# Kernel optimization log

Measured on AMD Instinct MI355X. Metric: run time of the kernel, lower is better.

The kernel has to match this reference:

```python
import jax, jax.numpy as jnp
import numpy as np

NUM_LAYERS = 3
H = 128          # hidden_dim
COMP_DIM = 128
PROT_DIM = 128
EPS = 1e-6


def setup_inputs() -> dict:
    key = jax.random.key(0)
    ks = jax.random.split(key, 20)
    B, Lc, Lp = 16, 512, 4096
    s = 0.05
    inp = {
        "comp_feat": jax.random.normal(ks[0], (B, Lc, COMP_DIM), jnp.float32),
        "comp_mask": jax.random.randint(ks[1], (B, Lc), 0, 2, jnp.int32),
        "prot_feat": jax.random.normal(ks[2], (B, Lp, PROT_DIM), jnp.float32),
        "prot_mask": jax.random.randint(ks[3], (B, Lp), 0, 2, jnp.int32),
        # per-layer params, stacked on leading layer axis. Linear(x) = x @ W + b
        # (W stored already transposed relative to torch's [out,in] layout).
        "Wc": jax.random.normal(ks[4], (NUM_LAYERS, COMP_DIM, H), jnp.float32) * s,
        "bc": jnp.zeros((NUM_LAYERS, H), jnp.float32),
        "Wp": jax.random.normal(ks[5], (NUM_LAYERS, PROT_DIM, H), jnp.float32) * s,
        "bp": jnp.zeros((NUM_LAYERS, H), jnp.float32),
        "Wbl": jax.random.normal(ks[6], (NUM_LAYERS, H, H), jnp.float32) * s,  # bilinear, no bias
        "Wac": jax.random.normal(ks[7], (NUM_LAYERS, H), jnp.float32) * s,    # Linear(H,1) weight
        "bac": jnp.zeros((NUM_LAYERS,), jnp.float32),
        "Wap": jax.random.normal(ks[8], (NUM_LAYERS, H), jnp.float32) * s,
        "bap": jnp.zeros((NUM_LAYERS,), jnp.float32),
        "Wcomb_c": jax.random.normal(ks[9], (NUM_LAYERS * H, H), jnp.float32) * s,
        "bcomb_c": jnp.zeros((H,), jnp.float32),
        "Wcomb_p": jax.random.normal(ks[10], (NUM_LAYERS * H, H), jnp.float32) * s,
        "bcomb_p": jnp.zeros((H,), jnp.float32),
    }
    return inp


def _masked_softmax(scores, mask):
    # faithful to torch: max over ALL entries (mask applied post-exp), +1e-6 denom
    m = jnp.max(scores, axis=-1, keepdims=True)
    e = jnp.exp(scores - m) * mask
    return e / (jnp.sum(e, axis=-1, keepdims=True) + EPS)


def reference(comp_feat, comp_mask, prot_feat, prot_mask,
              Wc, bc, Wp, bp, Wbl, Wac, bac, Wap, bap,
              Wcomb_c, bcomb_c, Wcomb_p, bcomb_p):
    cm = comp_mask.astype(jnp.float32)  # [B,Lc]
    pm = prot_mask.astype(jnp.float32)  # [B,Lp]
    comp_pooled_list, prot_pooled_list = [], []
    comp_context = prot_context = None
    for i in range(NUM_LAYERS):
        comp_proj = jnp.tanh(comp_feat @ Wc[i] + bc[i])   # [B,Lc,H]
        prot_proj = jnp.tanh(prot_feat @ Wp[i] + bp[i])   # [B,Lp,H]
        comp_bil = comp_proj @ Wbl[i]                      # [B,Lc,H]
        scores = jnp.einsum('bqh,bkh->bqk', comp_bil, prot_proj)  # [B,Lc,Lp]
        scores = scores * (cm[:, :, None] * pm[:, None, :])
        # broadcast-multiply-sum in torch == matmul; same math, efficient form
        comp_context = jnp.einsum('bqk,bkh->bqh', scores, prot_proj)  # [B,Lc,H]
        prot_context = jnp.einsum('bqk,bqh->bkh', scores, comp_proj)  # [B,Lp,H]
        cw = _masked_softmax(comp_context @ Wac[i] + bac[i], cm)  # [B,Lc]
        pw = _masked_softmax(prot_context @ Wap[i] + bap[i], pm)  # [B,Lp]
        comp_pooled_list.append(jnp.einsum('bqh,bq->bh', comp_proj, cw))
        prot_pooled_list.append(jnp.einsum('bkh,bk->bh', prot_proj, pw))
    comp_final = jnp.concatenate(comp_pooled_list, axis=1) @ Wcomb_c + bcomb_c
    prot_final = jnp.concatenate(prot_pooled_list, axis=1) @ Wcomb_p + bcomb_p
    # contexts returned are from the last layer (matches torch loop-variable leak)
    return (comp_final, prot_final, comp_context, prot_context)
```

## Files before the change

### kernel.cpp

```cpp
#include <hip/hip_runtime.h>
#include <math.h>

#define B_ 16
#define LC_ 512
#define LP_ 4096
#define H_ 128
#define HH_ (H_*H_)

typedef unsigned long long u64t;
typedef unsigned short u16t;
typedef __attribute__((ext_vector_type(8))) short bf16x8;
typedef __attribute__((ext_vector_type(4))) float f32x4;

__device__ __forceinline__ u16t f2bf(float f) {
    union { float f; unsigned u; } v; v.f = f;
    unsigned r = (v.u + 0x7FFFu + ((v.u >> 16) & 1u)) >> 16;
    return (u16t)r;
}
__device__ __forceinline__ float bf2f(u16t s) {
    union { unsigned u; float f; } v; v.u = ((unsigned)s) << 16; return v.f;
}
__device__ __forceinline__ float bflo(unsigned u) {
    union { unsigned u; float f; } v; v.u = u << 16; return v.f;
}
__device__ __forceinline__ float bfhi(unsigned u) {
    union { unsigned u; float f; } v; v.u = u & 0xffff0000u; return v.f;
}
__device__ __forceinline__ unsigned cvtpk2(float a, float b) {
    unsigned r;
    asm volatile("v_cvt_pk_bf16_f32 %0, %1, %2" : "=v"(r) : "v"(a), "v"(b));
    return r;
}
__device__ __forceinline__ float ftanh(float x) {
    float e = __expf(2.f * x);
    return fmaf(-2.f, __builtin_amdgcn_rcpf(e + 1.f), 1.f);
}
__device__ __forceinline__ bf16x8 ldfragS(const short* base, int r, int k, int stride) {
    const u64t* p = (const u64t*)(base + (size_t)r * stride + k);
    union { bf16x8 v; u64t q[2]; } u;
    u.q[0] = p[0]; u.q[1] = p[1];
    return u.v;
}
__device__ __forceinline__ bf16x8 ldfragG(const u16t* p) {
    union { bf16x8 v; uint4 q; } u;
    u.q = *(const uint4*)p;
    return u.v;
}

__device__ __forceinline__ void wprep_body(const float* __restrict__ src,
                                           u16t* __restrict__ h, u16t* __restrict__ l,
                                           int t) {
    const int n = t >> 1, k0 = (t & 1) * 64;
#pragma unroll 4
    for (int k = 0; k < 64; ++k) {
        float v = src[(size_t)(k0 + k) * H_ + n];
        u16t hh = f2bf(v);
        h[(size_t)n * H_ + k0 + k] = hh;
        l[(size_t)n * H_ + k0 + k] = f2bf(v - bf2f(hh));
    }
}

__global__ __launch_bounds__(256) void prep_k(const float* __restrict__ s0,
                                              const float* __restrict__ s1,
                                              const float* __restrict__ s2,
                                              u16t* __restrict__ hi, u16t* __restrict__ lo,
                                              float* __restrict__ zcp,
                                              float* __restrict__ zout) {
    const int bid = blockIdx.x, t = threadIdx.x;
    if (bid < 9) {
        const int grp = bid / 3, lay = bid % 3;
        const float* src = (grp == 0 ? s0 : grp == 1 ? s1 : s2) + (size_t)lay * HH_;
        wprep_body(src, hi + (size_t)bid * HH_, lo + (size_t)bid * HH_, t);
    } else {
        float4 zero = make_float4(0.f, 0.f, 0.f, 0.f);
        float4* z = (float4*)zcp;
        for (int j = t; j < 3072; j += 256) z[j] = zero;
        float4* z2 = (float4*)zout;
        for (int j = t; j < 1024; j += 256) z2[j] = zero;
    }
}

template<int ROWS>
__device__ __forceinline__ void stage_fp32(const float* __restrict__ X,
                                           short* __restrict__ Xs, int t) {
#pragma unroll
    for (int j = 0; j < ROWS / 16; ++j) {
        int lin = j * 512 + t;
        int row = lin >> 5, c4 = lin & 31;
        float4 v = ((const float4*)X)[lin];
        u64t pk = (u64t)cvtpk2(v.x, v.y) | ((u64t)cvtpk2(v.z, v.w) << 32);
        *(u64t*)(Xs + (size_t)row * 136 + c4 * 4) = pk;
    }
}
__device__ __forceinline__ void stage_bf16(const u16t* __restrict__ X,
                                           short* __restrict__ Xs, int t) {
#pragma unroll
    for (int j = 0; j < 4; ++j) {
        int lin = j * 512 + t;
        *(uint4*)(Xs + (lin >> 4) * 136 + (lin & 15) * 8) = ((const uint4*)X)[lin];
    }
}

template<int NRG, bool TANH, bool BF16OUT, bool LDSOUT>
__device__ __forceinline__ void gemm_core(const short* __restrict__ Xs,
                                          const u16t* __restrict__ Whi,
                                          const u16t* __restrict__ Wlo,
                                          const float* __restrict__ bias,
                                          const int* __restrict__ mrow,
                                          void* __restrict__ Yrow0,
                                          short* __restrict__ projLds, int t) {
    const int l = t & 63, w = t >> 6;
    const int lm = l & 15, lk = (l >> 4) * 8, lr = (l >> 4) * 4;
    const int wcol = w * 16;
    const size_t wrow = (size_t)(wcol + lm) * H_;
    f32x4 acc[NRG] = {};
#pragma unroll
    for (int ks = 0; ks < 128; ks += 32) {
        bf16x8 ah = ldfragG(Whi + wrow + ks + lk);
        bf16x8 al = ldfragG(Wlo + wrow + ks + lk);
#pragma unroll
        for (int rg = 0; rg < NRG; ++rg) {
            bf16x8 xb = ldfragS(Xs, rg * 16 + lm, ks + lk, 136);
            acc[rg] = __builtin_amdgcn_mfma_f32_16x16x32_bf16(ah, xb, acc[rg], 0, 0, 0);
            acc[rg] = __builtin_amdgcn_mfma_f32_16x16x32_bf16(al, xb, acc[rg], 0, 0, 0);
        }
    }
    if (LDSOUT) __syncthreads();
    const int col = wcol + lr;
    float4 bq = make_float4(0.f, 0.f, 0.f, 0.f);
    if (bias) bq = *(const float4*)(bias + col);
#pragma unroll
    for (int rg = 0; rg < NRG; ++rg) {
        const int row = rg * 16 + lm;
        float v0 = acc[rg][0] + bq.x, v1 = acc[rg][1] + bq.y;
        float v2 = acc[rg][2] + bq.z, v3 = acc[rg][3] + bq.w;
        if (TANH) { v0 = ftanh(v0); v1 = ftanh(v1); v2 = ftanh(v2); v3 = ftanh(v3); }
        if (mrow) {
            const float msc = (float)mrow[row];
            v0 *= msc; v1 *= msc; v2 *= msc; v3 *= msc;
        }
        if (BF16OUT) {
            u64t pk = (u64t)cvtpk2(v0, v1) | ((u64t)cvtpk2(v2, v3) << 32);
            *(u64t*)((u16t*)Yrow0 + (size_t)row * H_ + col) = pk;
            if (LDSOUT) *(u64t*)(projLds + (size_t)row * 136 + col) = pk;
        } else {
            float4 o; o.x = v0; o.y = v1; o.z = v2; o.w = v3;
            *(float4*)((float*)Yrow0 + (size_t)row * H_ + col) = o;
        }
    }
}

__global__ __launch_bounds__(512) void gemmB_k(const float* __restrict__ prot_feat,
                                               const float* __restrict__ comp_feat,
                                               const u16t* __restrict__ WHi,
                                               const u16t* __restrict__ WLo,
                                               const float* __restrict__ bp,
                                               const float* __restrict__ bc,
                                               u16t* __restrict__ prot_proj,
                                               u16t* __restrict__ comp_proj,
                                               u16t* __restrict__ comp_bil) {
    extern __shared__ __align__(16) short smem[];
    const int t = threadIdx.x, bx = blockIdx.x;
    if (bx < 128) {
        short* Xs = smem;
        short* Ys = smem + 64 * 136;
        const long row0 = (long)bx * 64;
        stage_fp32<64>(comp_feat + (size_t)row0 * H_, Xs, t);
        __syncthreads();
#pragma unroll 1
        for (int lay = 0; lay < 3; ++lay) {
            gemm_core<4, true, true, true>(Xs, WHi + (size_t)(3 + lay) * HH_,
                WLo + (size_t)(3 + lay) * HH_, bc + lay * H_, nullptr,
                comp_proj + ((size_t)lay * B_ * LC_ + row0) * H_, Ys, t);
            __syncthreads();
            gemm_core<4, false, true, false>(Ys, WHi + (size_t)(6 + lay) * HH_,
                WLo + (size_t)(6 + lay) * HH_, nullptr, nullptr,
                comp_bil + ((size_t)lay * B_ * LC_ + row0) * H_, nullptr, t);
        }
    } else {
        short* Xs = smem;
        const long row0 = (long)(bx - 128) * 128;
        stage_fp32<128>(prot_feat + (size_t)row0 * H_, Xs, t);
        __syncthreads();
#pragma unroll 1
        for (int lay = 0; lay < 3; ++lay)
            gemm_core<8, true, true, false>(Xs, WHi + (size_t)lay * HH_,
                WLo + (size_t)lay * HH_, bp + lay * H_, nullptr,
                prot_proj + ((size_t)lay * B_ * LP_ + row0) * H_, nullptr, t);
    }
}

__device__ __forceinline__ void stage64_bf(const u16t* __restrict__ src,
                                           const int* __restrict__ maskrow,
                                           short* __restrict__ dst, int t) {
    const int m = t & 31, kq = t >> 5;
#pragma unroll
    for (int p = 0; p < 2; ++p) {
        const int kc = p * 32 + kq * 4;
        u64t q[4];
#pragma unroll
        for (int r = 0; r < 4; ++r) {
            u64t v = *(const u64t*)(src + (size_t)(kc + r) * H_ + m * 4);
            if (maskrow && !maskrow[kc + r]) v = 0;
            q[r] = v;
        }
#pragma unroll
        for (int i = 0; i < 4; ++i) {
            u64t val = ((q[0] >> (16 * i)) & 0xffffull)
                     | (((q[1] >> (16 * i)) & 0xffffull) << 16)
                     | (((q[2] >> (16 * i)) & 0xffffull) << 32)
                     | (((q[3] >> (16 * i)) & 0xffffull) << 48);
            *(u64t*)(dst + (size_t)(4 * m + i) * 68 + kc) = val;
        }
    }
}

__global__ __launch_bounds__(256) void syrkC_k(const u16t* __restrict__ prot_proj,
                                               const u16t* __restrict__ comp_bil,
                                               const u16t* __restrict__ comp_proj,
                                               const int* __restrict__ prot_mask,
                                               const int* __restrict__ comp_mask,
                                               float* __restrict__ partP,
                                               float* __restrict__ partC) {
    __shared__ __align__(16) short smem[2 * 128 * 68];
    const int t = threadIdx.x;
    const int slice = blockIdx.x, b = blockIdx.y, z = blockIdx.z;
    const bool isP = z < 3;
    const int lay = isP ? z : z - 3;
    const u16t* Xl = isP ? prot_proj : comp_bil;
    const u16t* Yr = isP ? prot_proj : comp_proj;
    const int* mask = isP ? prot_mask : comp_mask;
    const int Kb = isP ? LP_ : LC_;
    const int rps = Kb >> 3;
    float* part = isP ? partP : partC;
    short* Xt = smem;
    short* Yt = isP ? smem : smem + 128 * 68;

    const int l = t & 63, w = t >> 6;
    const int qi = (w >> 1) * 64, qj = (w & 1) * 64;
    const int lm = l & 15, lk = (l >> 4) * 8, lr = (l >> 4) * 4;
    f32x4 acc[4][4] = {};
    const int chunks = rps >> 6;
    const size_t doff = ((size_t)lay * B_ + b) * Kb;
    const size_t moff = (size_t)b * Kb;

    for (int c = 0; c < chunks; ++c) {
        const int kbase = slice * rps + c * 64;
        stage64_bf(Xl + (doff + kbase) * H_, mask + moff + kbase, Xt, t);
        if (!isP) stage64_bf(Yr + (doff + kbase) * H_, nullptr, Yt, t);
        __syncthreads();
#pragma unroll
        for (int ks = 0; ks < 64; ks += 32) {
            bf16x8 af[4], bfr[4];
#pragma unroll
            for (int it = 0; it < 4; ++it) af[it] = ldfragS(Xt, qi + it * 16 + lm, ks + lk, 68);
#pragma unroll
            for (int jt = 0; jt < 4; ++jt) bfr[jt] = ldfragS(Yt, qj + jt * 16 + lm, ks + lk, 68);
#pragma unroll
            for (int it = 0; it < 4; ++it)
#pragma unroll
                for (int jt = 0; jt < 4; ++jt)
                    acc[it][jt] = __builtin_amdgcn_mfma_f32_16x16x32_bf16(
                        af[it], bfr[jt], acc[it][jt], 0, 0, 0);
        }
        __syncthreads();
    }

    float* pb = part + (((size_t)lay * 8 + slice) * B_ + b) * HH_;
#pragma unroll
    for (int it = 0; it < 4; ++it)
#pragma unroll
        for (int jt = 0; jt < 4; ++jt)
#pragma unroll
            for (int r = 0; r < 4; ++r)
                pb[(size_t)(qi + it * 16 + lr + r) * H_ + qj + jt * 16 + lm] = acc[it][jt][r];
}

__global__ __launch_bounds__(256) void reduceC_k(const float4* __restrict__ partP,
                                                 const float4* __restrict__ partC,
                                                 const float* __restrict__ Wac,
                                                 const float* __restrict__ Wap,
                                                 float* __restrict__ vc, float* __restrict__ vp,
                                                 u16t* __restrict__ MNhi, u16t* __restrict__ MNlo) {
    const int lay = blockIdx.y, z = blockIdx.z, t = threadIdx.x;
    const size_t quarter = (size_t)B_ * HH_ / 4;
    const float4* p = (z ? partC : partP) + (size_t)lay * 8 * quarter;
    const size_t idx = (size_t)blockIdx.x * 256 + t;
    float4 a = p[idx];
#pragma unroll
    for (int s = 1; s < 8; ++s) {
        float4 v = p[(size_t)s * quarter + idx];
        a.x += v.x; a.y += v.y; a.z += v.z; a.w += v.w;
    }
    const int b = (int)(idx >> 12);
    const int q = (int)(idx & 4095);
    const int row = q >> 5, c4 = q & 31;

    const float* Wv = (z ? Wap : Wac) + lay * H_;
    float4 w4 = ((const float4*)Wv)[c4];
    float s = a.x * w4.x + a.y * w4.y + a.z * w4.z + a.w * w4.w;
#pragma unroll
    for (int o = 16; o > 0; o >>= 1) s += __shfl_down(s, o, 32);
    if ((t & 31) == 0)
        (z ? vp : vc)[((size_t)lay * B_ + b) * H_ + row] = s;

    if (lay == 2) {
        u16t* hi = MNhi + ((size_t)z * B_ + b) * HH_;
        u16t* lo = MNlo + ((size_t)z * B_ + b) * HH_;
        const int colb = c4 * 4;
        float av[4] = {a.x, a.y, a.z, a.w};
#pragma unroll
        for (int j = 0; j < 4; ++j) {
            u16t hh = f2bf(av[j]);
            hi[(size_t)(colb + j) * H_ + row] = hh;
            lo[(size_t)(colb + j) * H_ + row] = f2bf(av[j] - bf2f(hh));
        }
    }
}

__global__ __launch_bounds__(256) void logitsC_k(const u16t* __restrict__ prot_proj,
                                                 const u16t* __restrict__ comp_bil,
                                                 const int* __restrict__ prot_mask,
                                                 const int* __restrict__ comp_mask,
                                                 const float* __restrict__ vp,
                                                 const float* __restrict__ vc,
                                                 const float* __restrict__ bap,
                                                 const float* __restrict__ bac,
                                                 float* __restrict__ logp,
                                                 float* __restrict__ logc) {
    const int zz = blockIdx.z;
    const bool isP = zz < 3;
    if (!isP && blockIdx.x >= LC_ / 256) return;
    const int lay = isP ? zz : zz - 3;
    const int b = blockIdx.y, t = threadIdx.x;
    const int n = isP ? LP_ : LC_;
    __shared__ float v[H_];
    if (t < 128) v[t] = (isP ? vp : vc)[((size_t)lay * B_ + b) * H_ + t];
    __syncthreads();
    const int r = blockIdx.x * 256 + t;
    const u16t* feat = (isP ? prot_proj : comp_bil) + (((size_t)lay * B_ + b) * n + r) * H_;
    const uint2* f2 = (const uint2*)feat;
    const float4* v4 = (const float4*)v;
    float acc = 0.f;
#pragma unroll
    for (int h4 = 0; h4 < 32; ++h4) {
        uint2 u = f2[h4];
        float4 c = v4[h4];
        acc = fmaf(bflo(u.x), c.x, acc); acc = fmaf(bfhi(u.x), c.y, acc);
        acc = fmaf(bflo(u.y), c.z, acc); acc = fmaf(bfhi(u.y), c.w, acc);
    }
    const int mk = (isP ? prot_mask : comp_mask)[(size_t)b * n + r];
    (isP ? logp : logc)[((size_t)lay * B_ + b) * n + r] = (float)mk * acc + (isP ? bap : bac)[lay];
}

__global__ __launch_bounds__(256) void softmaxC_k(const float* __restrict__ logp,
                                                  const float* __restrict__ logc,
                                                  const int* __restrict__ prot_mask,
                                                  const int* __restrict__ comp_mask,
                                                  float* __restrict__ pw,
                                                  float* __restrict__ cw) {
    const int b = blockIdx.x, zz = blockIdx.y, t = threadIdx.x;
    const bool isP = zz < 3;
    const int lay = isP ? zz : zz - 3;
    const int n = isP ? LP_ : LC_;
    const float* l = (isP ? logp : logc) + ((size_t)lay * B_ + b) * n;
    const int* mk = (isP ? prot_mask : comp_mask) + (size_t)b * n;
    float* ww = (isP ? pw : cw) + ((size_t)lay * B_ + b) * n;
    __shared__ float Es[LP_];
    __shared__ float red[4];

    float mx = -1e30f;
    for (int q = t; q < n; q += 256) { float x = l[q]; Es[q] = x; mx = fmaxf(mx, x); }
#pragma unroll
    for (int o = 32; o > 0; o >>= 1) mx = fmaxf(mx, __shfl_down(mx, o, 64));
    if ((t & 63) == 0) red[t >> 6] = mx;
    __syncthreads();
    float m = fmaxf(fmaxf(red[0], red[1]), fmaxf(red[2], red[3]));
    __syncthreads();

    float s = 0.f;
    for (int q = t; q < n; q += 256) {
        float e = __expf(Es[q] - m) * (float)mk[q];
        Es[q] = e;
        s += e;
    }
#pragma unroll
    for (int o = 32; o > 0; o >>= 1) s += __shfl_down(s, o, 64);
    if ((t & 63) == 0) red[t >> 6] = s;
    __syncthreads();
    float denom = red[0] + red[1] + red[2] + red[3] + 1e-6f;
    for (int q = t; q < n; q += 256) ww[q] = Es[q] / denom;
}

__global__ __launch_bounds__(256) void poolC_k(const u16t* __restrict__ prot_proj,
                                               const u16t* __restrict__ comp_proj,
                                               const float* __restrict__ pw,
                                               const float* __restrict__ cw,
                                               float* __restrict__ pp, float* __restrict__ cp) {
    const int zz = blockIdx.z;
    const bool isP = zz < 3;
    if (!isP && blockIdx.y >= 4) return;
    const int lay = isP ? zz : zz - 3;
    const int n = isP ? LP_ : LC_;
    const int chunk = isP ? 256 : 128;
    const int b = blockIdx.x, t = threadIdx.x;
    const int th = t & 63, tq = t >> 6;
    const int q0 = blockIdx.y * chunk;
    const u16t* pb = (isP ? prot_proj : comp_proj) + (((size_t)lay * B_ + b) * n + q0) * H_;
    const float* wb = (isP ? pw : cw) + ((size_t)lay * B_ + b) * n + q0;
    float a0 = 0.f, a1 = 0.f;
    for (int q = tq; q < chunk; q += 4) {
        float wq = wb[q];
        unsigned u = *(const unsigned*)(pb + (size_t)q * H_ + th * 2);
        a0 = fmaf(bflo(u), wq, a0);
        a1 = fmaf(bfhi(u), wq, a1);
    }
    float* ob = (isP ? pp : cp) + ((size_t)lay * B_ + b) * H_;
    atomicAdd(&ob[th * 2], a0);
    atomicAdd(&ob[th * 2 + 1], a1);
}

__global__ __launch_bounds__(512) void ctxC_k(const u16t* __restrict__ comp_bil,
                                              const u16t* __restrict__ prot_proj,
                                              const u16t* __restrict__ MNhi,
                                              const u16t* __restrict__ MNlo,
                                              const int* __restrict__ comp_mask,
                                              const int* __restrict__ prot_mask,
                                              float* __restrict__ out_cc,
                                              float* __restrict__ out_pc) {
    __shared__ __align__(16) short Xs[128 * 136];
    const int t = threadIdx.x, z = blockIdx.z;
    const bool isC = z < 16;
    if (isC && blockIdx.x >= LC_ / 128) return;
    const int b = isC ? z : z - 16;
    const int n = isC ? LC_ : LP_;
    const size_t rowoff = (size_t)b * n + (size_t)blockIdx.x * 128;
    const u16t* X = (isC ? comp_bil + (size_t)2 * B_ * LC_ * H_
                         : prot_proj + (size_t)2 * B_ * LP_ * H_) + rowoff * H_;
    const u16t* Whi = MNhi + ((size_t)(isC ? 0 : 1) * B_ + b) * HH_;
    const u16t* Wlo = MNlo + ((size_t)(isC ? 0 : 1) * B_ + b) * HH_;
    const int* mrow = (isC ? comp_mask : prot_mask) + rowoff;
    float* Y = (isC ? out_cc : out_pc) + rowoff * H_;
    stage_bf16(X, Xs, t);
    __syncthreads();
    gemm_core<8, false, false, false>(Xs, Whi, Wlo, nullptr, mrow, Y, nullptr, t);
}

__global__ void finalC_k(const float* __restrict__ cp, const float* __restrict__ pp,
                         const float* __restrict__ Wcc, const float* __restrict__ bcc,
                         const float* __restrict__ Wcp, const float* __restrict__ bcp,
                         float* __restrict__ out_cf, float* __restrict__ out_pf) {
    const int z = blockIdx.z;
    const float* pooled = z ? pp : cp;
    const float* Wcomb = z ? Wcp : Wcc;
    const float* bcomb = z ? bcp : bcc;
    float* out = z ? out_pf : out_cf;
    const int b = blockIdx.x, h = threadIdx.x, j0 = blockIdx.y * 64;
    float acc = (blockIdx.y == 0) ? bcomb[h] : 0.f;
#pragma unroll 4
    for (int j = 0; j < 64; ++j) {
        int jj = j0 + j;
        int lay = jj >> 7, hh = jj & 127;
        acc = fmaf(pooled[((size_t)lay * B_ + b) * H_ + hh], Wcomb[(size_t)jj * H_ + h], acc);
    }
    atomicAdd(&out[b * H_ + h], acc);
}

extern "C" void kernel_launch(void* const* d_in, const int* in_sizes, int n_in,
                              void* d_out, int out_size, void* d_ws, size_t ws_size,
                              hipStream_t stream) {
    const float* comp_feat = (const float*)d_in[0];
    const int*   comp_mask = (const int*)d_in[1];
    const float* prot_feat = (const float*)d_in[2];
    const int*   prot_mask = (const int*)d_in[3];
    const float* Wc      = (const float*)d_in[4];
    const float* bc      = (const float*)d_in[5];
    const float* Wp      = (const float*)d_in[6];
    const float* bp      = (const float*)d_in[7];
    const float* Wbl     = (const float*)d_in[8];
    const float* Wac     = (const float*)d_in[9];
    const float* bac     = (const float*)d_in[10];
    const float* Wap     = (const float*)d_in[11];
    const float* bap     = (const float*)d_in[12];
    const float* Wcomb_c = (const float*)d_in[13];
    const float* bcomb_c = (const float*)d_in[14];
    const float* Wcomb_p = (const float*)d_in[15];
    const float* bcomb_p = (const float*)d_in[16];

    u16t* prot_proj = (u16t*)d_ws;
    u16t* comp_proj = prot_proj + (size_t)3 * B_ * LP_ * H_;
    u16t* comp_bil  = comp_proj + (size_t)3 * B_ * LC_ * H_;
    u16t* WHi  = comp_bil + (size_t)3 * B_ * LC_ * H_;
    u16t* WLo  = WHi + (size_t)9 * HH_;
    u16t* MNhi = WLo + (size_t)9 * HH_;
    u16t* MNlo = MNhi + (size_t)32 * HH_;
    float* f = (float*)(MNlo + (size_t)32 * HH_);
    float* vc = f;    f += (size_t)3 * B_ * H_;
    float* vp = f;    f += (size_t)3 * B_ * H_;
    float* logc = f;  f += (size_t)3 * B_ * LC_;
    float* logp = f;  f += (size_t)3 * B_ * LP_;
    float* cw = f;    f += (size_t)3 * B_ * LC_;
    float* pw = f;    f += (size_t)3 * B_ * LP_;
    float* cp = f;    f += 3 * B_ * H_;
    float* pp = f;    f += 3 * B_ * H_;
    float* partP = pp + 3 * B_ * H_;
    float* partC = partP + (size_t)3 * 8 * B_ * HH_;

    float* out_cf = (float*)d_out;
    float* out_pf = out_cf + B_ * H_;
    float* out_cc = out_pf + B_ * H_;
    float* out_pc = out_cc + (size_t)B_ * LC_ * H_;

    prep_k<<<dim3(10), 256, 0, stream>>>(Wp, Wc, Wbl, WHi, WLo, cp, out_cf);
    gemmB_k<<<dim3(128 + 512), 512, 34816, stream>>>(
        prot_feat, comp_feat, WHi, WLo, bp, bc, prot_proj, comp_proj, comp_bil);
    syrkC_k<<<dim3(8, B_, 6), 256, 0, stream>>>(
        prot_proj, comp_bil, comp_proj, prot_mask, comp_mask, partP, partC);
    reduceC_k<<<dim3(256, 3, 2), 256, 0, stream>>>(
        (const float4*)partP, (const float4*)partC, Wac, Wap, vc, vp, MNhi, MNlo);
    logitsC_k<<<dim3(LP_ / 256, B_, 6), 256, 0, stream>>>(
        prot_proj, comp_bil, prot_mask, comp_mask, vp, vc, bap, bac, logp, logc);
    softmaxC_k<<<dim3(B_, 6), 256, 0, stream>>>(logp, logc, prot_mask, comp_mask, pw, cw);
    poolC_k<<<dim3(B_, 16, 6), 256, 0, stream>>>(prot_proj, comp_proj, pw, cw, pp, cp);
    ctxC_k<<<dim3(LP_ / 128, 1, 32), 512, 0, stream>>>(
        comp_bil, prot_proj, MNhi, MNlo, comp_mask, prot_mask, out_cc, out_pc);
    finalC_k<<<dim3(B_, 6, 2), 128, 0, stream>>>(
        cp, pp, Wcomb_c, bcomb_c, Wcomb_p, bcomb_p, out_cf, out_pf);
}
```

Baseline: 169.9 us.

## Drop low-part weight split in projections and reduce syrk K-slices

```diff
diff --git a/kernel.cpp b/kernel.cpp
--- a/kernel.cpp
+++ b/kernel.cpp
@@ -48,29 +48,26 @@
 }
 
 __device__ __forceinline__ void wprep_body(const float* __restrict__ src,
-                                           u16t* __restrict__ h, u16t* __restrict__ l,
-                                           int t) {
+                                           u16t* __restrict__ h, int t) {
     const int n = t >> 1, k0 = (t & 1) * 64;
 #pragma unroll 4
     for (int k = 0; k < 64; ++k) {
         float v = src[(size_t)(k0 + k) * H_ + n];
-        u16t hh = f2bf(v);
-        h[(size_t)n * H_ + k0 + k] = hh;
-        l[(size_t)n * H_ + k0 + k] = f2bf(v - bf2f(hh));
+        h[(size_t)n * H_ + k0 + k] = f2bf(v);
     }
 }
 
 __global__ __launch_bounds__(256) void prep_k(const float* __restrict__ s0,
                                               const float* __restrict__ s1,
                                               const float* __restrict__ s2,
-                                              u16t* __restrict__ hi, u16t* __restrict__ lo,
+                                              u16t* __restrict__ hi,
                                               float* __restrict__ zcp,
                                               float* __restrict__ zout) {
     const int bid = blockIdx.x, t = threadIdx.x;
     if (bid < 9) {
         const int grp = bid / 3, lay = bid % 3;
         const float* src = (grp == 0 ? s0 : grp == 1 ? s1 : s2) + (size_t)lay * HH_;
-        wprep_body(src, hi + (size_t)bid * HH_, lo + (size_t)bid * HH_, t);
+        wprep_body(src, hi + (size_t)bid * HH_, t);
     } else {
         float4 zero = make_float4(0.f, 0.f, 0.f, 0.f);
         float4* z = (float4*)zcp;
@@ -101,7 +98,7 @@
     }
 }
 
-template<int NRG, bool TANH, bool BF16OUT, bool LDSOUT>
+template<int NRG, bool TANH, bool BF16OUT, bool LDSOUT, bool HILO>
 __device__ __forceinline__ void gemm_core(const short* __restrict__ Xs,
                                           const u16t* __restrict__ Whi,
                                           const u16t* __restrict__ Wlo,
@@ -113,16 +110,22 @@
     const int lm = l & 15, lk = (l >> 4) * 8, lr = (l >> 4) * 4;
     const int wcol = w * 16;
     const size_t wrow = (size_t)(wcol + lm) * H_;
+    bf16x8 wh[4], wl[4];
+#pragma unroll
+    for (int i = 0; i < 4; ++i) wh[i] = ldfragG(Whi + wrow + i * 32 + lk);
+    if (HILO) {
+#pragma unroll
+        for (int i = 0; i < 4; ++i) wl[i] = ldfragG(Wlo + wrow + i * 32 + lk);
+    }
     f32x4 acc[NRG] = {};
 #pragma unroll
-    for (int ks = 0; ks < 128; ks += 32) {
-        bf16x8 ah = ldfragG(Whi + wrow + ks + lk);
-        bf16x8 al = ldfragG(Wlo + wrow + ks + lk);
+    for (int i = 0; i < 4; ++i) {
 #pragma unroll
         for (int rg = 0; rg < NRG; ++rg) {
-            bf16x8 xb = ldfragS(Xs, rg * 16 + lm, ks + lk, 136);
-            acc[rg] = __builtin_amdgcn_mfma_f32_16x16x32_bf16(ah, xb, acc[rg], 0, 0, 0);
-            acc[rg] = __builtin_amdgcn_mfma_f32_16x16x32_bf16(al, xb, acc[rg], 0, 0, 0);
+            bf16x8 xb = ldfragS(Xs, rg * 16 + lm, i * 32 + lk, 136);
+            acc[rg] = __builtin_amdgcn_mfma_f32_16x16x32_bf16(wh[i], xb, acc[rg], 0, 0, 0);
+            if (HILO)
+                acc[rg] = __builtin_amdgcn_mfma_f32_16x16x32_bf16(wl[i], xb, acc[rg], 0, 0, 0);
         }
     }
     if (LDSOUT) __syncthreads();
@@ -153,7 +156,6 @@
 __global__ __launch_bounds__(512) void gemmB_k(const float* __restrict__ prot_feat,
                                                const float* __restrict__ comp_feat,
                                                const u16t* __restrict__ WHi,
-                                               const u16t* __restrict__ WLo,
                                                const float* __restrict__ bp,
                                                const float* __restrict__ bc,
                                                u16t* __restrict__ prot_proj,
@@ -169,12 +171,12 @@
         __syncthreads();
 #pragma unroll 1
         for (int lay = 0; lay < 3; ++lay) {
-            gemm_core<4, true, true, true>(Xs, WHi + (size_t)(3 + lay) * HH_,
-                WLo + (size_t)(3 + lay) * HH_, bc + lay * H_, nullptr,
+            gemm_core<4, true, true, true, false>(Xs, WHi + (size_t)(3 + lay) * HH_,
+                nullptr, bc + lay * H_, nullptr,
                 comp_proj + ((size_t)lay * B_ * LC_ + row0) * H_, Ys, t);
             __syncthreads();
-            gemm_core<4, false, true, false>(Ys, WHi + (size_t)(6 + lay) * HH_,
-                WLo + (size_t)(6 + lay) * HH_, nullptr, nullptr,
+            gemm_core<4, false, true, false, false>(Ys, WHi + (size_t)(6 + lay) * HH_,
+                nullptr, nullptr, nullptr,
                 comp_bil + ((size_t)lay * B_ * LC_ + row0) * H_, nullptr, t);
         }
     } else {
@@ -184,8 +186,8 @@
         __syncthreads();
 #pragma unroll 1
         for (int lay = 0; lay < 3; ++lay)
-            gemm_core<8, true, true, false>(Xs, WHi + (size_t)lay * HH_,
-                WLo + (size_t)lay * HH_, bp + lay * H_, nullptr,
+            gemm_core<8, true, true, false, false>(Xs, WHi + (size_t)lay * HH_,
+                nullptr, bp + lay * H_, nullptr,
                 prot_proj + ((size_t)lay * B_ * LP_ + row0) * H_, nullptr, t);
     }
 }
@@ -214,6 +216,9 @@
         }
     }
 }
+
+#define SL_P 4
+#define SL_C 2
 
 __global__ __launch_bounds__(256) void syrkC_k(const u16t* __restrict__ prot_proj,
                                                const u16t* __restrict__ comp_bil,
@@ -226,12 +231,14 @@
     const int t = threadIdx.x;
     const int slice = blockIdx.x, b = blockIdx.y, z = blockIdx.z;
     const bool isP = z < 3;
+    const int slices = isP ? SL_P : SL_C;
+    if (slice >= slices) return;
     const int lay = isP ? z : z - 3;
     const u16t* Xl = isP ? prot_proj : comp_bil;
     const u16t* Yr = isP ? prot_proj : comp_proj;
     const int* mask = isP ? prot_mask : comp_mask;
     const int Kb = isP ? LP_ : LC_;
-    const int rps = Kb >> 3;
+    const int rps = Kb / slices;
     float* part = isP ? partP : partC;
     short* Xt = smem;
     short* Yt = isP ? smem : smem + 128 * 68;
@@ -266,7 +273,7 @@
         __syncthreads();
     }
 
-    float* pb = part + (((size_t)lay * 8 + slice) * B_ + b) * HH_;
+    float* pb = part + (((size_t)lay * slices + slice) * B_ + b) * HH_;
 #pragma unroll
     for (int it = 0; it < 4; ++it)
 #pragma unroll
@@ -283,12 +290,12 @@
                                                  float* __restrict__ vc, float* __restrict__ vp,
                                                  u16t* __restrict__ MNhi, u16t* __restrict__ MNlo) {
     const int lay = blockIdx.y, z = blockIdx.z, t = threadIdx.x;
+    const int slices = z ? SL_C : SL_P;
     const size_t quarter = (size_t)B_ * HH_ / 4;
-    const float4* p = (z ? partC : partP) + (size_t)lay * 8 * quarter;
+    const float4* p = (z ? partC : partP) + (size_t)lay * slices * quarter;
     const size_t idx = (size_t)blockIdx.x * 256 + t;
     float4 a = p[idx];
-#pragma unroll
-    for (int s = 1; s < 8; ++s) {
+    for (int s = 1; s < slices; ++s) {
         float4 v = p[(size_t)s * quarter + idx];
         a.x += v.x; a.y += v.y; a.z += v.z; a.w += v.w;
     }
@@ -443,7 +450,7 @@
     float* Y = (isC ? out_cc : out_pc) + rowoff * H_;
     stage_bf16(X, Xs, t);
     __syncthreads();
-    gemm_core<8, false, false, false>(Xs, Whi, Wlo, nullptr, mrow, Y, nullptr, t);
+    gemm_core<8, false, false, false, true>(Xs, Whi, Wlo, nullptr, mrow, Y, nullptr, t);
 }
 
 __global__ void finalC_k(const float* __restrict__ cp, const float* __restrict__ pp,
@@ -491,8 +498,7 @@
     u16t* comp_proj = prot_proj + (size_t)3 * B_ * LP_ * H_;
     u16t* comp_bil  = comp_proj + (size_t)3 * B_ * LC_ * H_;
     u16t* WHi  = comp_bil + (size_t)3 * B_ * LC_ * H_;
-    u16t* WLo  = WHi + (size_t)9 * HH_;
-    u16t* MNhi = WLo + (size_t)9 * HH_;
+    u16t* MNhi = WHi + (size_t)9 * HH_;
     u16t* MNlo = MNhi + (size_t)32 * HH_;
     float* f = (float*)(MNlo + (size_t)32 * HH_);
     float* vc = f;    f += (size_t)3 * B_ * H_;
@@ -504,17 +510,17 @@
     float* cp = f;    f += 3 * B_ * H_;
     float* pp = f;    f += 3 * B_ * H_;
     float* partP = pp + 3 * B_ * H_;
-    float* partC = partP + (size_t)3 * 8 * B_ * HH_;
+    float* partC = partP + (size_t)3 * SL_P * B_ * HH_;
 
     float* out_cf = (float*)d_out;
     float* out_pf = out_cf + B_ * H_;
     float* out_cc = out_pf + B_ * H_;
     float* out_pc = out_cc + (size_t)B_ * LC_ * H_;
 
-    prep_k<<<dim3(10), 256, 0, stream>>>(Wp, Wc, Wbl, WHi, WLo, cp, out_cf);
+    prep_k<<<dim3(10), 256, 0, stream>>>(Wp, Wc, Wbl, WHi, cp, out_cf);
     gemmB_k<<<dim3(128 + 512), 512, 34816, stream>>>(
-        prot_feat, comp_feat, WHi, WLo, bp, bc, prot_proj, comp_proj, comp_bil);
-    syrkC_k<<<dim3(8, B_, 6), 256, 0, stream>>>(
+        prot_feat, comp_feat, WHi, bp, bc, prot_proj, comp_proj, comp_bil);
+    syrkC_k<<<dim3(SL_P, B_, 6), 256, 0, stream>>>(
         prot_proj, comp_bil, comp_proj, prot_mask, comp_mask, partP, partC);
     reduceC_k<<<dim3(256, 3, 2), 256, 0, stream>>>(
         (const float4*)partP, (const float4*)partC, Wac, Wap, vc, vp, MNhi, MNlo);
```

Result: slower. 179.7 us (+5.8%).
